# Kernel tuning notes

Measured on AMD Instinct MI355X. Metric: run time of the kernel, lower is better.

The kernel has to match this reference:

```python
import jax, jax.numpy as jnp
import numpy as np

H = 128   # hidden_size
E = 300   # embedding_dim
VOC = 32000
B, TP, TC = 8, 160, 160
D2 = 2 * H  # bidirectional feature dim


def gru_dir(x, Wih, Whh, bih, bhh, reverse):
    # x: [B,T,I] -> hidden states [B,T,Hs]; torch GRU gate order (r,z,n)
    Hs = Whh.shape[1]
    xg = jnp.einsum('bti,gi->btg', x, Wih) + bih  # [B,T,3Hs]
    if reverse:
        xg = xg[:, ::-1]
    def step(h, xt):
        gh = h @ Whh.T + bhh
        xr, xz, xn = jnp.split(xt, 3, axis=-1)
        hr, hz, hn = jnp.split(gh, 3, axis=-1)
        r = jax.nn.sigmoid(xr + hr)
        z = jax.nn.sigmoid(xz + hz)
        n = jnp.tanh(xn + r * hn)
        h = (1.0 - z) * n + z * h
        return h, h
    h0 = jnp.zeros((x.shape[0], Hs), x.dtype)
    _, hs = jax.lax.scan(step, h0, jnp.swapaxes(xg, 0, 1))
    hs = jnp.swapaxes(hs, 0, 1)
    if reverse:
        hs = hs[:, ::-1]
    return hs


def bigru(x, Wf, Uf, bif, bhf, Wb, Ub, bib, bhb):
    return jnp.concatenate([
        gru_dir(x, Wf, Uf, bif, bhf, False),
        gru_dir(x, Wb, Ub, bib, bhb, True)], axis=-1)


def setup_inputs() -> dict:
    key = jax.random.key(0)
    ks = iter(jax.random.split(key, 64))
    def rn(shape, s=0.05):
        return jax.random.normal(next(ks), shape, jnp.float32) * s
    inp = {}
    inp['text_a'] = jax.random.randint(next(ks), (B, TP), 0, VOC)
    inp['text_b'] = jax.random.randint(next(ks), (B, TC), 0, VOC)
    inp['emb'] = rn((VOC, E), 0.1)
    for pfx, ins in [('p', E), ('c', E), ('a', 6 * D2)]:
        for d in ('f', 'b'):
            inp[pfx + '_Wih_' + d] = rn((3 * H, ins))
            inp[pfx + '_Whh_' + d] = rn((3 * H, H))
            inp[pfx + '_bih_' + d] = jnp.zeros((3 * H,), jnp.float32)
            inp[pfx + '_bhh_' + d] = jnp.zeros((3 * H,), jnp.float32)
    inp['Wc1'] = rn((H, D2)); inp['Wc2'] = rn((H, D2)); inp['Vc'] = rn((H,))
    inp['Wb'] = rn((D2, D2))
    inp['Wd'] = rn((H, D2)); inp['Vd'] = rn((H,))
    inp['Wm'] = rn((H, D2)); inp['Vm'] = rn((H,))
    inp['Ws'] = rn((H, D2)); inp['Vs'] = rn((H,))
    inp['Wp'] = rn((H, D2)); inp['Vp'] = rn((H,))
    inp['W1'] = rn((H, D2)); inp['W2'] = rn((H, D2)); inp['Vv'] = rn((H,))
    inp['Wout'] = rn((2, D2)); inp['bout'] = jnp.zeros((2,), jnp.float32)
    return inp


def _forward(text_a, text_b, emb,
             p_Wih_f, p_Whh_f, p_bih_f, p_bhh_f, p_Wih_b, p_Whh_b, p_bih_b, p_bhh_b,
             c_Wih_f, c_Whh_f, c_bih_f, c_bhh_f, c_Wih_b, c_Whh_b, c_bih_b, c_bhh_b,
             a_Wih_f, a_Whh_f, a_bih_f, a_bhh_f, a_Wih_b, a_Whh_b, a_bih_b, a_bhh_b,
             Wc1, Wc2, Vc, Wb, Wd, Vd, Wm, Vm, Ws, Vs, Wp, Vp, W1, W2, Vv, Wout, bout):
    hp = bigru(emb[text_a], p_Wih_f, p_Whh_f, p_bih_f, p_bhh_f,
               p_Wih_b, p_Whh_b, p_bih_b, p_bhh_b)          # [B,Tp,2H]
    hc = bigru(emb[text_b], c_Wih_f, c_Whh_f, c_bih_f, c_bhh_f,
               c_Wih_b, c_Whh_b, c_bih_b, c_bhh_b)          # [B,Tc,2H]
    # concat (additive) attention: [B,Tc,Tp,H]
    s = jnp.tanh((hp @ Wc1.T)[:, None] + (hc @ Wc2.T)[:, :, None])
    a_cat = jax.nn.softmax(s @ Vc, axis=2)                   # [B,Tc,Tp]
    concat_rep = jnp.einsum('bct,btd->bcd', a_cat, hp)
    # bilinear attention
    a_bil = jax.nn.softmax(jnp.einsum('bcd,btd->bct', hc, hp @ Wb.T), axis=2)
    bil_rep = jnp.einsum('bct,btd->bcd', a_bil, hp)
    # dot / minus attention on [B,Tc,Tp,2H] broadcasts
    hp4 = hp[:, None]; hc4 = hc[:, :, None]
    a_dot = jax.nn.softmax(jnp.tanh((hp4 * hc4) @ Wd.T) @ Vd, axis=2)
    dot_rep = jnp.einsum('bct,btd->bcd', a_dot, hp)
    a_min = jax.nn.softmax(jnp.tanh((hp4 - hc4) @ Wm.T) @ Vm, axis=2)
    minus_rep = jnp.einsum('bct,btd->bcd', a_min, hp)
    # self attention on hc: [B,Tc,Tc,2H]
    a_self = jax.nn.softmax(jnp.tanh((hc[:, None] * hc[:, :, None]) @ Ws.T) @ Vs, axis=2)
    self_rep = jnp.einsum('bct,btd->bcd', a_self, hc)
    agg_in = jnp.concatenate([hc, self_rep, concat_rep, dot_rep, bil_rep, minus_rep], axis=-1)
    agg = bigru(agg_in, a_Wih_f, a_Whh_f, a_bih_f, a_bhh_f,
                a_Wih_b, a_Whh_b, a_bih_b, a_bhh_b)          # [B,Tc,2H]
    # pooled passage rep
    ap = jax.nn.softmax(jnp.tanh(hp @ Wp.T) @ Vp, axis=-1)   # [B,Tp]
    rp = jnp.einsum('bt,btd->bd', ap, hp)                    # [B,2H]
    # final attention over aggregation (note: no tanh, faithful to source)
    sc = (agg @ W1.T + (rp @ W2.T)[:, None]) @ Vv            # [B,Tc]
    ac = jax.nn.softmax(sc, axis=-1)
    rc = jnp.einsum('bc,bcd->bd', ac, agg)                   # [B,2H]
    return rc @ Wout.T + bout                                # [B,2] logits


def reference(text_a, text_b, emb,
              p_Wih_f, p_Whh_f, p_bih_f, p_bhh_f, p_Wih_b, p_Whh_b, p_bih_b, p_bhh_b,
              c_Wih_f, c_Whh_f, c_bih_f, c_bhh_f, c_Wih_b, c_Whh_b, c_bih_b, c_bhh_b,
              a_Wih_f, a_Whh_f, a_bih_f, a_bhh_f, a_Wih_b, a_Whh_b, a_bih_b, a_bhh_b,
              Wc1, Wc2, Vc, Wb, Wd, Vd, Wm, Vm, Ws, Vs, Wp, Vp, W1, W2, Vv, Wout, bout):
    return _forward(text_a, text_b, emb,
                    p_Wih_f, p_Whh_f, p_bih_f, p_bhh_f, p_Wih_b, p_Whh_b, p_bih_b, p_bhh_b,
                    c_Wih_f, c_Whh_f, c_bih_f, c_bhh_f, c_Wih_b, c_Whh_b, c_bih_b, c_bhh_b,
                    a_Wih_f, a_Whh_f, a_bih_f, a_bhh_f, a_Wih_b, a_Whh_b, a_bih_b, a_bhh_b,
                    Wc1, Wc2, Vc, Wb, Wd, Vd, Wm, Vm, Ws, Vs, Wp, Vp, W1, W2, Vv, Wout, bout)
```

## Files before the change

### kernel.cpp

```cpp
#include <hip/hip_runtime.h>

#define BB 8
#define TT 160
#define EE 300
#define HH 128
#define D2 256
#define G3 384
#define PSTR 40
#define HBP 900

typedef __attribute__((ext_vector_type(8))) short bf16x8;
typedef __attribute__((ext_vector_type(4))) float floatx4;

__device__ inline float fsigmoid(float x){ return 1.f/(1.f+__expf(-x)); }
__device__ inline float ftanh(float x){ return 2.f*fsigmoid(2.f*x) - 1.f; }

__device__ inline void split2(float x, unsigned short& hi, unsigned short& lo){
  unsigned ux = __float_as_uint(x);
  hi = (unsigned short)(ux>>16);
  float r = x - __uint_as_float(ux & 0xFFFF0000u);
  lo = (unsigned short)(__float_as_uint(r)>>16);
}

__device__ inline float quad_sum(float x){
  x += __uint_as_float(__builtin_amdgcn_mov_dpp(__float_as_uint(x), 0xB1, 0xF, 0xF, true));
  x += __uint_as_float(__builtin_amdgcn_mov_dpp(__float_as_uint(x), 0x4E, 0xF, 0xF, true));
  return x;
}

__global__ __launch_bounds__(256) void k_embed(const int* ta, const int* tb,
    const float* emb, float* ep, float* ec){
  const int idx = blockIdx.x*256 + threadIdx.x;
  const int per = BB*TT*EE;
  if (idx < per){
    const int e = idx % EE, bt = idx / EE;
    ep[idx] = emb[(long)ta[bt]*EE + e];
  } else {
    const int j = idx - per;
    const int e = j % EE, bt = j / EE;
    ec[j] = emb[(long)tb[bt]*EE + e];
  }
}

__global__ __launch_bounds__(256) void k_splitarr(const float* a, const float* b, int n,
    unsigned short* ahi, unsigned short* alo, unsigned short* bhi, unsigned short* blo){
  const int idx = blockIdx.x*256 + threadIdx.x;
  if (idx < n){
    split2(a[idx], ahi[idx], alo[idx]);
    split2(b[idx], bhi[idx], blo[idx]);
  }
}

struct SplitJob { const float* W; unsigned short* hi; unsigned short* lo; int n; int K; int Kp; };
struct SplitJobs { SplitJob j[14]; };

__global__ __launch_bounds__(256) void k_splitw(SplitJobs jobs){
  const SplitJob J = jobs.j[blockIdx.z];
  const int idx = blockIdx.x*256 + threadIdx.x;
  if (idx >= J.n) return;
  const int row = idx / J.Kp, k = idx - row*J.Kp;
  const float v = (k < J.K) ? J.W[(long)row*J.K + k] : 0.f;
  split2(v, J.hi[idx], J.lo[idx]);
}

struct GemmSJob {
  const float* A; const unsigned short* Whi; const unsigned short* Wlo; const float* bias;
  float* C; int N; int K; int Kp;
};
struct GemmSJobs { GemmSJob j[6]; };

__global__ __launch_bounds__(256) void k_gemmS(GemmSJobs jobs){
  const GemmSJob J = jobs.j[blockIdx.z];
  const int tid = threadIdx.x;
  const int lane = tid & 63, w = tid >> 6;
  const int l15 = lane & 15, q = lane >> 4;
  const int n0 = blockIdx.x * 64;
  if (n0 >= J.N) return;
  const int K = J.K, Kp = J.Kp;
  const long mrow = blockIdx.y*64 + w*16 + l15;
  const float* Arow = J.A + mrow*K;
  floatx4 acc[4];
  #pragma unroll
  for (int t=0;t<4;t++) acc[t] = (floatx4)0.f;
  const int nch = (K+31)>>5;
  for (int kc=0; kc<nch; kc++){
    const int k0 = kc<<5;
    const int kb = k0 + q*8;
    float av[8];
    if (k0+32 <= K){
      const floatx4 a0 = *(const floatx4*)(Arow+kb);
      const floatx4 a1 = *(const floatx4*)(Arow+kb+4);
      av[0]=a0[0];av[1]=a0[1];av[2]=a0[2];av[3]=a0[3];
      av[4]=a1[0];av[5]=a1[1];av[6]=a1[2];av[7]=a1[3];
    } else {
      #pragma unroll
      for (int j=0;j<8;j++){ const int k=kb+j; av[j] = (k<K)? Arow[k] : 0.f; }
    }
    union { bf16x8 v; unsigned short u[8]; } ahi, alo;
    #pragma unroll
    for (int j=0;j<8;j++) split2(av[j], ahi.u[j], alo.u[j]);
    #pragma unroll
    for (int t=0;t<4;t++){
      const int n = n0 + t*16 + l15;
      const long wo = (long)n*Kp + kb;
      union { bf16x8 v; uint4 d; } whi, wlo;
      whi.d = *(const uint4*)(J.Whi + wo);
      wlo.d = *(const uint4*)(J.Wlo + wo);
      acc[t] = __builtin_amdgcn_mfma_f32_16x16x32_bf16(ahi.v, whi.v, acc[t], 0,0,0);
      acc[t] = __builtin_amdgcn_mfma_f32_16x16x32_bf16(ahi.v, wlo.v, acc[t], 0,0,0);
      acc[t] = __builtin_amdgcn_mfma_f32_16x16x32_bf16(alo.v, whi.v, acc[t], 0,0,0);
    }
  }
  const long rbase = blockIdx.y*64 + w*16 + q*4;
  #pragma unroll
  for (int t=0;t<4;t++){
    const int n = n0 + t*16 + l15;
    const float bv = J.bias ? J.bias[n] : 0.f;
    #pragma unroll
    for (int r=0;r<4;r++)
      J.C[(rbase+r)*(long)J.N + n] = acc[t][r] + bv;
  }
}

struct GemmPJob {
  const unsigned short* Ahi; const unsigned short* Alo;
  const unsigned short* Whi; const unsigned short* Wlo; const float* bias;
  float* C; int N; int Kp;
};
struct GemmPJobs { GemmPJob j[6]; };

__global__ __launch_bounds__(256) void k_gemmSS(GemmPJobs jobs){
  const GemmPJob J = jobs.j[blockIdx.z];
  const int tid = threadIdx.x;
  const int lane = tid & 63, w = tid >> 6;
  const int l15 = lane & 15, q = lane >> 4;
  const int n0 = blockIdx.x * 64;
  if (n0 >= J.N) return;
  const int Kp = J.Kp;
  const long arow = (blockIdx.y*64 + w*16 + l15) * (long)Kp;
  floatx4 acc[4];
  #pragma unroll
  for (int t=0;t<4;t++) acc[t] = (floatx4)0.f;
  const int nch = Kp >> 5;
  for (int kc=0; kc<nch; kc++){
    const int kb = (kc<<5) + q*8;
    union { bf16x8 v; uint4 d; } ahi, alo;
    ahi.d = *(const uint4*)(J.Ahi + arow + kb);
    alo.d = *(const uint4*)(J.Alo + arow + kb);
    #pragma unroll
    for (int t=0;t<4;t++){
      const int n = n0 + t*16 + l15;
      const long wo = (long)n*Kp + kb;
      union { bf16x8 v; uint4 d; } whi, wlo;
      whi.d = *(const uint4*)(J.Whi + wo);
      wlo.d = *(const uint4*)(J.Wlo + wo);
      acc[t] = __builtin_amdgcn_mfma_f32_16x16x32_bf16(ahi.v, whi.v, acc[t], 0,0,0);
      acc[t] = __builtin_amdgcn_mfma_f32_16x16x32_bf16(ahi.v, wlo.v, acc[t], 0,0,0);
      acc[t] = __builtin_amdgcn_mfma_f32_16x16x32_bf16(alo.v, whi.v, acc[t], 0,0,0);
    }
  }
  const long rbase = blockIdx.y*64 + w*16 + q*4;
  #pragma unroll
  for (int t=0;t<4;t++){
    const int n = n0 + t*16 + l15;
    const float bv = J.bias ? J.bias[n] : 0.f;
    #pragma unroll
    for (int r=0;r<4;r++)
      J.C[(rbase+r)*(long)J.N + n] = acc[t][r] + bv;
  }
}

struct GruJob { const float* xg; const float* Whh; const float* bhh; float* out; int ocol; int rev; };
struct GruJobs { GruJob j[4]; };

__global__ __launch_bounds__(512,1) void k_gru(GruJobs jobs){
  const GruJob J = jobs.j[blockIdx.y];
  const int bi = blockIdx.x;
  const int tid = threadIdx.x;
  const int j = tid >> 2, p = tid & 3;
  const int rot = p*8;
  const int base = p*32;
  __shared__ float xgt[16][G3];
  __shared__ float hbuf[16][HBP];
  __shared__ float hcur[2][HH];
  const float* r0 = J.Whh + (long)j*HH + base;
  const float* z0 = J.Whh + (long)(HH+j)*HH + base;
  const float* n0 = J.Whh + (long)(2*HH+j)*HH + base;
  #define LDV(gp,i) (*(const floatx4*)((gp) + (((i)*4 + rot) & 31)))
  floatx4 wr0=LDV(r0,0), wr1=LDV(r0,1), wr2=LDV(r0,2), wr3=LDV(r0,3),
          wr4=LDV(r0,4), wr5=LDV(r0,5), wr6=LDV(r0,6), wr7=LDV(r0,7);
  floatx4 wz0=LDV(z0,0), wz1=LDV(z0,1), wz2=LDV(z0,2), wz3=LDV(z0,3),
          wz4=LDV(z0,4), wz5=LDV(z0,5), wz6=LDV(z0,6), wz7=LDV(z0,7);
  floatx4 wn0=LDV(n0,0), wn1=LDV(n0,1), wn2=LDV(n0,2), wn3=LDV(n0,3),
          wn4=LDV(n0,4), wn5=LDV(n0,5), wn6=LDV(n0,6), wn7=LDV(n0,7);
  #undef LDV
  asm volatile("" : "+v"(wr0), "+v"(wr1), "+v"(wr2), "+v"(wr3));
  asm volatile("" : "+v"(wr4), "+v"(wr5), "+v"(wr6), "+v"(wr7));
  asm volatile("" : "+v"(wz0), "+v"(wz1), "+v"(wz2), "+v"(wz3));
  asm volatile("" : "+v"(wz4), "+v"(wz5), "+v"(wz6), "+v"(wz7));
  asm volatile("" : "+v"(wn0), "+v"(wn1), "+v"(wn2), "+v"(wn3));
  asm volatile("" : "+v"(wn4), "+v"(wn5), "+v"(wn6), "+v"(wn7));
  const float bhr = J.bhh[j];
  const float bhz = J.bhh[HH+j];
  const float bhn = J.bhh[2*HH+j];
  if (tid < 256) ((float*)hcur)[tid] = 0.f;
  float hreg = 0.f;
  __syncthreads();

  for (int s0=0; s0<TT; s0+=16){
    #pragma unroll
    for (int r=0;r<3;r++){
      const int i = r*512 + tid;
      const int row = i/96, c4 = i - row*96;
      const int tt = J.rev ? (TT-1-(s0+row)) : (s0+row);
      *(floatx4*)&xgt[row][c4*4] = *(const floatx4*)(J.xg + ((long)bi*TT + tt)*G3 + c4*4);
    }
    __syncthreads();
    for (int si=0; si<16; si++){
      const int s = s0 + si;
      const int buf = s & 1;
      float ar=0.f, az=0.f, an=0.f;
      #define ACC(i) { \
        const floatx4 h4 = *(const floatx4*)&hcur[buf][base + (((i)*4 + rot) & 31)]; \
        ar += wr##i[0]*h4[0] + wr##i[1]*h4[1] + wr##i[2]*h4[2] + wr##i[3]*h4[3]; \
        az += wz##i[0]*h4[0] + wz##i[1]*h4[1] + wz##i[2]*h4[2] + wz##i[3]*h4[3]; \
        an += wn##i[0]*h4[0] + wn##i[1]*h4[1] + wn##i[2]*h4[2] + wn##i[3]*h4[3]; }
      ACC(0) ACC(1) ACC(2) ACC(3) ACC(4) ACC(5) ACC(6) ACC(7)
      #undef ACC
      const float cxr = xgt[si][j];
      const float cxz = xgt[si][HH+j];
      const float cxn = xgt[si][2*HH+j];
      ar = quad_sum(ar);
      az = quad_sum(az);
      an = quad_sum(an);
      const float gr = fsigmoid(cxr + ar + bhr);
      const float gz = fsigmoid(cxz + az + bhz);
      const float gn = ftanh  (cxn + gr*(an + bhn));
      const float h = (1.f-gz)*gn + gz*hreg;
      hreg = h;
      if (p==0){
        hcur[1-buf][j] = h;
        hbuf[si][j] = h;
      }
      __syncthreads();
    }
    {
      const int row = tid >> 5, c4 = tid & 31;
      const int tt = J.rev ? (TT-1-(s0+row)) : (s0+row);
      *(floatx4*)(J.out + ((long)bi*TT + tt)*D2 + J.ocol + c4*4) = *(const floatx4*)&hbuf[row][c4*4];
    }
  }
}

__device__ inline float block_softmax160(float s, int tid, float* red){
  float m = s;
  #pragma unroll
  for (int o=32;o>0;o>>=1) m = fmaxf(m, __shfl_xor(m,o));
  if ((tid&63)==0) red[tid>>6] = m;
  __syncthreads();
  m = fmaxf(fmaxf(red[0],red[1]), fmaxf(red[2],red[3]));
  const float p = (tid<TT) ? __expf(s-m) : 0.f;
  float t = p;
  #pragma unroll
  for (int o=32;o>0;o>>=1) t += __shfl_xor(t,o);
  if ((tid&63)==0) red[4+(tid>>6)] = t;
  __syncthreads();
  const float sum = red[4]+red[5]+red[6]+red[7];
  return p / sum;
}

struct PairJob { const unsigned short* Phi; const unsigned short* Plo;
                 const float* Q; const float* W; const float* V; float* a_out; };

__global__ __launch_bounds__(512) void k_pairattn(PairJob j0, PairJob j1){
  const PairJob J = blockIdx.z ? j1 : j0;
  const int b = blockIdx.y, c0 = blockIdx.x*2;
  const int tid = threadIdx.x;
  const int lane = tid & 63, w = tid >> 6;
  const int l15 = lane & 15, q = lane >> 4;
  __shared__ unsigned short Pb[2*2*160*PSTR];
  __shared__ float Qs[2][D2];
  __shared__ float sc_sh[2][TT];
  __shared__ float red[16];
  {
    const int row = tid >> 8, col = tid & 255;
    Qs[row][col] = J.Q[((long)b*TT + c0 + row)*D2 + col];
  }
  if (tid < 2*TT) ((float*)sc_sh)[tid] = 0.f;
  const long pbase = (long)b*TT*D2;

  const unsigned short* srcp[5];
  unsigned short* dstp[5];
  #pragma unroll
  for (int r=0;r<5;r++){
    const int idx = tid + r*512;
    const int hl = (idx >= 1280) ? 1 : 0;
    const int e4 = idx - hl*1280;
    const int st = e4 >> 3, sd4 = e4 & 7;
    srcp[r] = (hl ? J.Plo : J.Phi) + pbase + (long)st*D2 + sd4*4;
    dstp[r] = &Pb[((0*2 + hl)*160 + st)*PSTR + sd4*4];
  }
  uint2 stg[5];
  #pragma unroll
  for (int r=0;r<5;r++) stg[r] = *(const uint2*)(srcp[r]);
  const float* Wbase = J.W + (long)(w*16 + l15)*D2;
  floatx4 wv0 = *(const floatx4*)(Wbase + q*8);
  floatx4 wv1 = *(const floatx4*)(Wbase + q*8 + 4);
  #pragma unroll
  for (int r=0;r<5;r++) *(uint2*)(dstp[r]) = stg[r];
  __syncthreads();

  floatx4 acc0[10], acc1[10];
  #pragma unroll
  for (int nt=0;nt<10;nt++){ acc0[nt] = (floatx4)0.f; acc1[nt] = (floatx4)0.f; }

  for (int kc=0; kc<8; kc++){
    const floatx4 wc0 = wv0, wc1 = wv1;
    if (kc < 7){
      wv0 = *(const floatx4*)(Wbase + (kc+1)*32 + q*8);
      wv1 = *(const floatx4*)(Wbase + (kc+1)*32 + q*8 + 4);
      #pragma unroll
      for (int r=0;r<5;r++) stg[r] = *(const uint2*)(srcp[r] + (kc+1)*32);
    }
    const int d0 = kc*32 + q*8;
    const floatx4 q00 = *(const floatx4*)&Qs[0][d0];
    const floatx4 q01 = *(const floatx4*)&Qs[0][d0+4];
    const floatx4 q10 = *(const floatx4*)&Qs[1][d0];
    const floatx4 q11 = *(const floatx4*)&Qs[1][d0+4];
    union { bf16x8 v; unsigned short u[8]; } ah0, al0, ah1, al1;
    #pragma unroll
    for (int j=0;j<4;j++){
      split2(wc0[j]*q00[j], ah0.u[j],   al0.u[j]);
      split2(wc1[j]*q01[j], ah0.u[4+j], al0.u[4+j]);
      split2(wc0[j]*q10[j], ah1.u[j],   al1.u[j]);
      split2(wc1[j]*q11[j], ah1.u[4+j], al1.u[4+j]);
    }
    const int buf = kc & 1;
    #pragma unroll
    for (int nt=0;nt<10;nt++){
      const int t = nt*16 + l15;
      union { bf16x8 v; } bh, bl;
      bh.v = *(const bf16x8*)&Pb[((buf*2+0)*160 + t)*PSTR + q*8];
      bl.v = *(const bf16x8*)&Pb[((buf*2+1)*160 + t)*PSTR + q*8];
      acc0[nt] = __builtin_amdgcn_mfma_f32_16x16x32_bf16(ah0.v, bh.v, acc0[nt], 0,0,0);
      acc0[nt] = __builtin_amdgcn_mfma_f32_16x16x32_bf16(ah0.v, bl.v, acc0[nt], 0,0,0);
      acc0[nt] = __builtin_amdgcn_mfma_f32_16x16x32_bf16(al0.v, bh.v, acc0[nt], 0,0,0);
      acc1[nt] = __builtin_amdgcn_mfma_f32_16x16x32_bf16(ah1.v, bh.v, acc1[nt], 0,0,0);
      acc1[nt] = __builtin_amdgcn_mfma_f32_16x16x32_bf16(ah1.v, bl.v, acc1[nt], 0,0,0);
      acc1[nt] = __builtin_amdgcn_mfma_f32_16x16x32_bf16(al1.v, bh.v, acc1[nt], 0,0,0);
    }
    if (kc < 7){
      const int nbuf = 1 - buf;
      #pragma unroll
      for (int r=0;r<5;r++) *(uint2*)(dstp[r] + nbuf*(2*160*PSTR)) = stg[r];
      __syncthreads();
    }
  }

  float vreg[4];
  #pragma unroll
  for (int r=0;r<4;r++) vreg[r] = J.V[w*16 + q*4 + r];
  #pragma unroll
  for (int nt=0;nt<10;nt++){
    float p0 = 0.f, p1 = 0.f;
    #pragma unroll
    for (int r=0;r<4;r++){
      p0 += vreg[r]*ftanh(acc0[nt][r]);
      p1 += vreg[r]*ftanh(acc1[nt][r]);
    }
    p0 += __shfl_xor(p0,16); p0 += __shfl_xor(p0,32);
    p1 += __shfl_xor(p1,16); p1 += __shfl_xor(p1,32);
    if (q==0){
      atomicAdd(&sc_sh[0][nt*16 + l15], p0);
      atomicAdd(&sc_sh[1][nt*16 + l15], p1);
    }
  }
  __syncthreads();
  {
    const int row = tid >> 8, t_ = tid & 255;
    float s = (t_ < TT) ? sc_sh[row][t_] : -INFINITY;
    float m = s;
    #pragma unroll
    for (int o=32;o>0;o>>=1) m = fmaxf(m, __shfl_xor(m,o));
    if (lane==0) red[w] = m;
    __syncthreads();
    m = fmaxf(fmaxf(red[row*4+0],red[row*4+1]), fmaxf(red[row*4+2],red[row*4+3]));
    const float p = (t_ < TT) ? __expf(s-m) : 0.f;
    float su = p;
    #pragma unroll
    for (int o=32;o>0;o>>=1) su += __shfl_xor(su,o);
    if (lane==0) red[8+w] = su;
    __syncthreads();
    const float ssum = red[8+row*4+0]+red[8+row*4+1]+red[8+row*4+2]+red[8+row*4+3];
    if (t_ < TT) J.a_out[((long)b*TT + c0 + row)*TT + t_] = p/ssum;
  }
}

struct AddJob { const float* up; const float* uc; const float* V; float sgn; float* a_out; };

__global__ __launch_bounds__(256) void k_addattn(AddJob j0, AddJob j1){
  const AddJob J = blockIdx.z ? j1 : j0;
  const int b = blockIdx.y, c0 = blockIdx.x*16, tid = threadIdx.x;
  const int ci = tid >> 4, tj = tid & 15;
  __shared__ float ucc[16][132];
  __shared__ float up_sh[16][132];
  __shared__ float vv[HH];
  __shared__ float sc[16][TT];
  if (tid < HH) vv[tid] = J.V[tid];
  for (int i = tid; i < 16*HH; i += 256){
    const int cc = i >> 7, k = i & 127;
    ucc[cc][k] = J.sgn * J.uc[((long)b*TT + c0 + cc)*HH + k];
  }
  __syncthreads();
  for (int tch = 0; tch < 10; tch++){
    for (int i = tid; i < 16*HH; i += 256){
      const int tt = i >> 7, k = i & 127;
      up_sh[tt][k] = J.up[((long)b*TT + tch*16 + tt)*HH + k];
    }
    __syncthreads();
    float a0 = 0.f;
    #pragma unroll 4
    for (int k = 0; k < HH; k += 4){
      const floatx4 u4 = *(const floatx4*)&up_sh[tj][k];
      const floatx4 c4 = *(const floatx4*)&ucc[ci][k];
      a0 += vv[k]*ftanh(u4[0]+c4[0]) + vv[k+1]*ftanh(u4[1]+c4[1])
          + vv[k+2]*ftanh(u4[2]+c4[2]) + vv[k+3]*ftanh(u4[3]+c4[3]);
    }
    sc[ci][tch*16 + tj] = a0;
    __syncthreads();
  }
  float m = -INFINITY;
  float sv[10];
  #pragma unroll
  for (int u = 0; u < 10; u++){ sv[u] = sc[ci][tj + 16*u]; m = fmaxf(m, sv[u]); }
  #pragma unroll
  for (int o = 8; o >= 1; o >>= 1) m = fmaxf(m, __shfl_xor(m, o));
  float ssum = 0.f;
  #pragma unroll
  for (int u = 0; u < 10; u++){ sv[u] = __expf(sv[u] - m); ssum += sv[u]; }
  #pragma unroll
  for (int o = 8; o >= 1; o >>= 1) ssum += __shfl_xor(ssum, o);
  const float inv = 1.f / ssum;
  float* ao = J.a_out + ((long)b*TT + c0 + ci)*TT + tj;
  #pragma unroll
  for (int u = 0; u < 10; u++) ao[16*u] = sv[u]*inv;
}

__global__ __launch_bounds__(256) void k_bilattn(const float* hc, const float* hpWb, float* a_out){
  const int b = blockIdx.y, c = blockIdx.x, tid = threadIdx.x;
  __shared__ float hcc[D2];
  __shared__ float red[8];
  if (tid < D2) hcc[tid] = hc[((long)b*TT + c)*D2 + tid];
  __syncthreads();
  float s = -INFINITY;
  if (tid < TT){
    const float* pr = hpWb + ((long)b*TT + tid)*D2;
    float a0 = 0.f;
    #pragma unroll 4
    for (int k=0;k<D2;k++) a0 += hcc[k]*pr[k];
    s = a0;
  }
  const float a = block_softmax160(s, tid, red);
  if (tid < TT) a_out[((long)b*TT + c)*TT + tid] = a;
}

__global__ __launch_bounds__(256) void k_rep(const float* hp, const float* hc,
    const float* acat, const float* abil, const float* adot, const float* amin, const float* aself,
    float* aggin){
  const int b = blockIdx.y, c = blockIdx.x, tid = threadIdx.x;
  __shared__ float a5[5][TT];
  {
    const long base = ((long)b*TT + c)*TT;
    for (int i=tid;i<5*TT;i+=256){
      const int which = i/TT, t = i - which*TT;
      const float* p = which==0? acat : which==1? abil : which==2? adot : which==3? amin : aself;
      a5[which][t] = p[base + t];
    }
  }
  __syncthreads();
  const float* hpb = hp + (long)b*TT*D2 + tid;
  const float* hcb = hc + (long)b*TT*D2 + tid;
  float r0=0.f,r1=0.f,r2=0.f,r3=0.f,r4=0.f;
  for (int t=0;t<TT;t++){
    const float vp = hpb[(long)t*D2];
    const float vc = hcb[(long)t*D2];
    r0 += a5[0][t]*vp;
    r1 += a5[1][t]*vp;
    r2 += a5[2][t]*vp;
    r3 += a5[3][t]*vp;
    r4 += a5[4][t]*vc;
  }
  float* o = aggin + ((long)b*TT + c)*(6*D2);
  o[tid]        = hc[((long)b*TT + c)*D2 + tid];
  o[D2 + tid]   = r4;
  o[2*D2 + tid] = r0;
  o[3*D2 + tid] = r2;
  o[4*D2 + tid] = r1;
  o[5*D2 + tid] = r3;
}

__global__ __launch_bounds__(256) void k_tail1(const float* upP, const float* Vp,
    const float* hp, float* rp){
  const int b = blockIdx.x, tid = threadIdx.x;
  __shared__ float vv[HH];
  __shared__ float ap_sh[TT];
  __shared__ float red[8];
  if (tid<HH) vv[tid] = Vp[tid];
  __syncthreads();
  float s = -INFINITY;
  if (tid<TT){
    const float* ur = upP + ((long)b*TT + tid)*HH;
    float a0=0.f;
    #pragma unroll 4
    for (int k=0;k<HH;k++) a0 += vv[k]*ftanh(ur[k]);
    s = a0;
  }
  const float a = block_softmax160(s, tid, red);
  if (tid<TT) ap_sh[tid] = a;
  __syncthreads();
  float acc = 0.f;
  const float* hpb = hp + (long)b*TT*D2 + tid;
  for (int t=0;t<TT;t++) acc += ap_sh[t]*hpb[(long)t*D2];
  rp[b*D2 + tid] = acc;
}

__global__ __launch_bounds__(256) void k_tail2(const float* aggW1, const float* agg, const float* rp,
    const float* W2, const float* Vv, const float* Wout, const float* bout,
    float* out){
  const int b = blockIdx.x, tid = threadIdx.x;
  __shared__ float rps[D2];
  __shared__ float rpw[HH];
  __shared__ float ac_sh[TT];
  __shared__ float rc_sh[D2];
  __shared__ float red[8];
  if (tid < D2) rps[tid] = rp[b*D2 + tid];
  __syncthreads();
  if (tid < HH){
    float a0=0.f;
    const float* wr2 = W2 + (long)tid*D2;
    for (int d=0; d<D2; d+=4){
      const floatx4 w4 = *(const floatx4*)(wr2 + d);
      a0 += w4[0]*rps[d] + w4[1]*rps[d+1] + w4[2]*rps[d+2] + w4[3]*rps[d+3];
    }
    rpw[tid] = a0;
  }
  __syncthreads();
  float s = -INFINITY;
  if (tid < TT){
    const float* ar = aggW1 + ((long)b*TT + tid)*HH;
    float a0=0.f;
    for (int k=0;k<HH;k++) a0 += Vv[k]*(ar[k] + rpw[k]);
    s = a0;
  }
  const float a = block_softmax160(s, tid, red);
  if (tid < TT) ac_sh[tid] = a;
  __syncthreads();
  float rc=0.f;
  const float* ab = agg + (long)b*TT*D2 + tid;
  for (int t=0;t<TT;t++) rc += ac_sh[t]*ab[(long)t*D2];
  rc_sh[tid] = rc;
  __syncthreads();
  if (tid < 2){
    float o = bout[tid];
    const float* wr = Wout + (long)tid*D2;
    for (int d=0; d<D2; d++) o += wr[d]*rc_sh[d];
    out[b*2 + tid] = o;
  }
}

extern "C" void kernel_launch(void* const* d_in, const int* in_sizes, int n_in,
                              void* d_out, int out_size, void* d_ws, size_t ws_size,
                              hipStream_t stream){
  (void)in_sizes; (void)n_in; (void)out_size; (void)ws_size;
  const int* ta = (const int*)d_in[0];
  const int* tb = (const int*)d_in[1];
  const float* emb = (const float*)d_in[2];
  #define F32(i) ((const float*)d_in[i])

  float* ws = (float*)d_ws;
  float* ep    = ws;
  float* ec    = ep    + 384000;
  float* xg_pf = ec    + 384000;
  float* xg_pb = xg_pf + 491520;
  float* xg_cf = xg_pb + 491520;
  float* xg_cb = xg_cf + 491520;
  float* hp    = xg_cb + 491520;
  float* hc    = hp    + 327680;
  float* up1   = hc    + 327680;
  float* uc2   = up1   + 163840;
  float* ump   = uc2   + 163840;
  float* umc   = ump   + 163840;
  float* upP   = umc   + 163840;
  float* hpWb  = upP   + 163840;
  float* acat  = hpWb  + 327680;
  float* abil  = acat  + 204800;
  float* adot  = abil  + 204800;
  float* amin  = adot  + 204800;
  float* aself = amin  + 204800;
  float* aggin = aself + 204800;
  float* rp    = aggin + 1966080;
  unsigned short* hp_hi = (unsigned short*)(rp + 2048);
  unsigned short* hp_lo = hp_hi + 327680;
  unsigned short* hc_hi = hp_lo + 327680;
  unsigned short* hc_lo = hc_hi + 327680;
  unsigned short* wsp = hc_lo + 327680;
  unsigned short* w3h  = wsp;             unsigned short* w3l  = w3h  + 122880;
  unsigned short* w7h  = w3l  + 122880;   unsigned short* w7l  = w7h  + 122880;
  unsigned short* w11h = w7l  + 122880;   unsigned short* w11l = w11h + 122880;
  unsigned short* w15h = w11l + 122880;   unsigned short* w15l = w15h + 122880;
  unsigned short* w27h = w15l + 122880;   unsigned short* w27l = w27h + 32768;
  unsigned short* w28h = w27l + 32768;    unsigned short* w28l = w28h + 32768;
  unsigned short* w33h = w28l + 32768;    unsigned short* w33l = w33h + 32768;
  unsigned short* w37h = w33l + 32768;    unsigned short* w37l = w37h + 32768;
  unsigned short* w30h = w37l + 32768;    unsigned short* w30l = w30h + 65536;
  unsigned short* w19h = w30l + 65536;    unsigned short* w19l = w19h + 589824;
  unsigned short* w23h = w19l + 589824;   unsigned short* w23l = w23h + 589824;
  unsigned short* w39h = w23l + 589824;   unsigned short* w39l = w39h + 32768;
  unsigned short* eph  = w39l + 32768;    unsigned short* epl  = eph + 409600;
  unsigned short* ech  = epl + 409600;    unsigned short* ecl  = ech + 409600;
  unsigned short* agh  = (unsigned short*)up1;
  unsigned short* agl  = agh + 1966080;
  float* xg_af = xg_pf;
  float* xg_ab = xg_pb;
  float* agg   = xg_cf;
  float* aggW1 = xg_cb;

  k_embed<<<dim3(3000), dim3(256), 0, stream>>>(ta, tb, emb, ep, ec);
  SplitJobs sj = {};
  sj.j[0]  = {F32(3),  w3h,  w3l,  122880, 300, 320};
  sj.j[1]  = {F32(7),  w7h,  w7l,  122880, 300, 320};
  sj.j[2]  = {F32(11), w11h, w11l, 122880, 300, 320};
  sj.j[3]  = {F32(15), w15h, w15l, 122880, 300, 320};
  sj.j[4]  = {F32(27), w27h, w27l, 32768,  256, 256};
  sj.j[5]  = {F32(28), w28h, w28l, 32768,  256, 256};
  sj.j[6]  = {F32(33), w33h, w33l, 32768,  256, 256};
  sj.j[7]  = {F32(37), w37h, w37l, 32768,  256, 256};
  sj.j[8]  = {F32(30), w30h, w30l, 65536,  256, 256};
  sj.j[9]  = {F32(19), w19h, w19l, 589824, 1536, 1536};
  sj.j[10] = {F32(23), w23h, w23l, 589824, 1536, 1536};
  sj.j[11] = {F32(39), w39h, w39l, 32768,  256, 256};
  sj.j[12] = {ep,      eph,  epl,  409600, 300, 320};
  sj.j[13] = {ec,      ech,  ecl,  409600, 300, 320};
  k_splitw<<<dim3(2304,1,14), dim3(256), 0, stream>>>(sj);

  GemmPJobs ja = {};
  ja.j[0] = {eph, epl, w3h,  w3l,  F32(5),  xg_pf, 384, 320};
  ja.j[1] = {eph, epl, w7h,  w7l,  F32(9),  xg_pb, 384, 320};
  ja.j[2] = {ech, ecl, w11h, w11l, F32(13), xg_cf, 384, 320};
  ja.j[3] = {ech, ecl, w15h, w15l, F32(17), xg_cb, 384, 320};
  k_gemmSS<<<dim3(6,20,4), dim3(256), 0, stream>>>(ja);

  GruJobs gj = {};
  gj.j[0] = {xg_pf, F32(4),  F32(6),  hp, 0,   0};
  gj.j[1] = {xg_pb, F32(8),  F32(10), hp, 128, 1};
  gj.j[2] = {xg_cf, F32(12), F32(14), hc, 0,   0};
  gj.j[3] = {xg_cb, F32(16), F32(18), hc, 128, 1};
  k_gru<<<dim3(8,4), dim3(512), 0, stream>>>(gj);

  k_splitarr<<<dim3(1280), dim3(256), 0, stream>>>(hp, hc, 327680, hp_hi, hp_lo, hc_hi, hc_lo);

  GemmPJobs jb = {};
  jb.j[0] = {hp_hi, hp_lo, w27h, w27l, nullptr, up1,  128, 256};
  jb.j[1] = {hc_hi, hc_lo, w28h, w28l, nullptr, uc2,  128, 256};
  jb.j[2] = {hp_hi, hp_lo, w33h, w33l, nullptr, ump,  128, 256};
  jb.j[3] = {hc_hi, hc_lo, w33h, w33l, nullptr, umc,  128, 256};
  jb.j[4] = {hp_hi, hp_lo, w37h, w37l, nullptr, upP,  128, 256};
  jb.j[5] = {hp_hi, hp_lo, w30h, w30l, nullptr, hpWb, 256, 256};
  k_gemmSS<<<dim3(4,20,6), dim3(256), 0, stream>>>(jb);

  PairJob pd  = {hp_hi, hp_lo, hc, F32(31), F32(32), adot};
  PairJob psf = {hc_hi, hc_lo, hc, F32(35), F32(36), aself};
  k_pairattn<<<dim3(80,8,2), dim3(512), 0, stream>>>(pd, psf);

  AddJob ac_ = {up1, uc2, F32(29),  1.f, acat};
  AddJob am_ = {ump, umc, F32(34), -1.f, amin};
  k_addattn<<<dim3(10,8,2), dim3(256), 0, stream>>>(ac_, am_);

  k_bilattn<<<dim3(160,8), dim3(256), 0, stream>>>(hc, hpWb, abil);

  k_tail1<<<dim3(8), dim3(256), 0, stream>>>(upP, F32(38), hp, rp);

  k_rep<<<dim3(160,8), dim3(256), 0, stream>>>(hp, hc, acat, abil, adot, amin, aself, aggin);

  SplitJobs sja = {};
  sja.j[0] = {aggin, agh, agl, 1966080, 1536, 1536};
  k_splitw<<<dim3(7680,1,1), dim3(256), 0, stream>>>(sja);

  GemmPJobs jc = {};
  jc.j[0] = {agh, agl, w19h, w19l, F32(21), xg_af, 384, 1536};
  jc.j[1] = {agh, agl, w23h, w23l, F32(25), xg_ab, 384, 1536};
  k_gemmSS<<<dim3(6,20,2), dim3(256), 0, stream>>>(jc);

  GruJobs gja = {};
  gja.j[0] = {xg_af, F32(20), F32(22), agg, 0,   0};
  gja.j[1] = {xg_ab, F32(24), F32(26), agg, 128, 1};
  k_gru<<<dim3(8,2), dim3(512), 0, stream>>>(gja);

  GemmSJobs jd = {};
  jd.j[0] = {agg, w39h, w39l, nullptr, aggW1, 128, 256, 256};
  k_gemmS<<<dim3(2,20,1), dim3(256), 0, stream>>>(jd);

  k_tail2<<<dim3(8), dim3(256), 0, stream>>>(aggW1, agg, rp, F32(40), F32(41), F32(42), F32(43),
                                             (float*)d_out);
  #undef F32
}
```

Measured before the change: 821.1 us.

## Run GRU recurrence on MFMA with split-bf16 weights, batching all sequences per block

The GRU recurrent matvec moves from per-thread fp32 FMAs, with one block per batch element, to bf16x3 split MFMA 16x16x32. One block now processes all 8 batch rows as an MFMA M-dimension padded to 16, and the hidden state is kept as hi/lo bf16 in LDS. Recurrent weights are pre-split in the existing split kernel, and the grid shrinks from 8x4 to 1x4 blocks. This removes redundant per-batch weight register loads and uses matrix cores, but it serialises all batches onto fewer CUs and wastes half the MFMA rows. It also adds uncoalesced per-step global loads of xg and a large dummy LDS pad that forces one block per CU.

```diff
diff --git a/kernel.cpp b/kernel.cpp
--- a/kernel.cpp
+++ b/kernel.cpp
@@ -7,7 +7,6 @@
 #define D2 256
 #define G3 384
 #define PSTR 40
-#define HBP 900
 
 typedef __attribute__((ext_vector_type(8))) short bf16x8;
 typedef __attribute__((ext_vector_type(4))) float floatx4;
@@ -20,12 +19,6 @@
   hi = (unsigned short)(ux>>16);
   float r = x - __uint_as_float(ux & 0xFFFF0000u);
   lo = (unsigned short)(__float_as_uint(r)>>16);
-}
-
-__device__ inline float quad_sum(float x){
-  x += __uint_as_float(__builtin_amdgcn_mov_dpp(__float_as_uint(x), 0xB1, 0xF, 0xF, true));
-  x += __uint_as_float(__builtin_amdgcn_mov_dpp(__float_as_uint(x), 0x4E, 0xF, 0xF, true));
-  return x;
 }
 
 __global__ __launch_bounds__(256) void k_embed(const int* ta, const int* tb,
@@ -52,7 +45,7 @@
 }
 
 struct SplitJob { const float* W; unsigned short* hi; unsigned short* lo; int n; int K; int Kp; };
-struct SplitJobs { SplitJob j[14]; };
+struct SplitJobs { SplitJob j[20]; };
 
 __global__ __launch_bounds__(256) void k_splitw(SplitJobs jobs){
   const SplitJob J = jobs.j[blockIdx.z];
@@ -170,85 +163,96 @@
   }
 }
 
-struct GruJob { const float* xg; const float* Whh; const float* bhh; float* out; int ocol; int rev; };
+struct GruJob { const float* xg; const unsigned short* whh; const unsigned short* whl;
+                const float* bhh; float* out; int ocol; int rev; };
 struct GruJobs { GruJob j[4]; };
 
 __global__ __launch_bounds__(512,1) void k_gru(GruJobs jobs){
   const GruJob J = jobs.j[blockIdx.y];
-  const int bi = blockIdx.x;
   const int tid = threadIdx.x;
-  const int j = tid >> 2, p = tid & 3;
-  const int rot = p*8;
-  const int base = p*32;
-  __shared__ float xgt[16][G3];
-  __shared__ float hbuf[16][HBP];
-  __shared__ float hcur[2][HH];
-  const float* r0 = J.Whh + (long)j*HH + base;
-  const float* z0 = J.Whh + (long)(HH+j)*HH + base;
-  const float* n0 = J.Whh + (long)(2*HH+j)*HH + base;
-  #define LDV(gp,i) (*(const floatx4*)((gp) + (((i)*4 + rot) & 31)))
-  floatx4 wr0=LDV(r0,0), wr1=LDV(r0,1), wr2=LDV(r0,2), wr3=LDV(r0,3),
-          wr4=LDV(r0,4), wr5=LDV(r0,5), wr6=LDV(r0,6), wr7=LDV(r0,7);
-  floatx4 wz0=LDV(z0,0), wz1=LDV(z0,1), wz2=LDV(z0,2), wz3=LDV(z0,3),
-          wz4=LDV(z0,4), wz5=LDV(z0,5), wz6=LDV(z0,6), wz7=LDV(z0,7);
-  floatx4 wn0=LDV(n0,0), wn1=LDV(n0,1), wn2=LDV(n0,2), wn3=LDV(n0,3),
-          wn4=LDV(n0,4), wn5=LDV(n0,5), wn6=LDV(n0,6), wn7=LDV(n0,7);
-  #undef LDV
-  asm volatile("" : "+v"(wr0), "+v"(wr1), "+v"(wr2), "+v"(wr3));
-  asm volatile("" : "+v"(wr4), "+v"(wr5), "+v"(wr6), "+v"(wr7));
-  asm volatile("" : "+v"(wz0), "+v"(wz1), "+v"(wz2), "+v"(wz3));
-  asm volatile("" : "+v"(wz4), "+v"(wz5), "+v"(wz6), "+v"(wz7));
-  asm volatile("" : "+v"(wn0), "+v"(wn1), "+v"(wn2), "+v"(wn3));
-  asm volatile("" : "+v"(wn4), "+v"(wn5), "+v"(wn6), "+v"(wn7));
-  const float bhr = J.bhh[j];
-  const float bhz = J.bhh[HH+j];
-  const float bhn = J.bhh[2*HH+j];
-  if (tid < 256) ((float*)hcur)[tid] = 0.f;
-  float hreg = 0.f;
-  __syncthreads();
-
-  for (int s0=0; s0<TT; s0+=16){
-    #pragma unroll
-    for (int r=0;r<3;r++){
-      const int i = r*512 + tid;
-      const int row = i/96, c4 = i - row*96;
-      const int tt = J.rev ? (TT-1-(s0+row)) : (s0+row);
-      *(floatx4*)&xgt[row][c4*4] = *(const floatx4*)(J.xg + ((long)bi*TT + tt)*G3 + c4*4);
+  const int w = tid >> 6;
+  const int lane = tid & 63;
+  const int l15 = lane & 15, q = lane >> 4;
+  const int j = w*16 + l15;
+  __shared__ __align__(16) unsigned short Hhi[2][16][136];
+  __shared__ __align__(16) unsigned short Hlo[2][16][136];
+  __shared__ float ldspad[16384];
+  if (tid == 0) ((volatile float*)ldspad)[0] = 0.f;
+  for (int i = tid; i < 2*16*136/2; i += 512){
+    ((unsigned*)Hhi)[i] = 0u;
+    ((unsigned*)Hlo)[i] = 0u;
+  }
+  const long jb0 = (long)j*128 + q*8;
+  #define LBV(p,g,kc) (*(const bf16x8*)((p) + (long)(g)*16384 + jb0 + (kc)*32))
+  bf16x8 h00=LBV(J.whh,0,0), h01=LBV(J.whh,0,1), h02=LBV(J.whh,0,2), h03=LBV(J.whh,0,3);
+  bf16x8 h10=LBV(J.whh,1,0), h11=LBV(J.whh,1,1), h12=LBV(J.whh,1,2), h13=LBV(J.whh,1,3);
+  bf16x8 h20=LBV(J.whh,2,0), h21=LBV(J.whh,2,1), h22=LBV(J.whh,2,2), h23=LBV(J.whh,2,3);
+  bf16x8 l00=LBV(J.whl,0,0), l01=LBV(J.whl,0,1), l02=LBV(J.whl,0,2), l03=LBV(J.whl,0,3);
+  bf16x8 l10=LBV(J.whl,1,0), l11=LBV(J.whl,1,1), l12=LBV(J.whl,1,2), l13=LBV(J.whl,1,3);
+  bf16x8 l20=LBV(J.whl,2,0), l21=LBV(J.whl,2,1), l22=LBV(J.whl,2,2), l23=LBV(J.whl,2,3);
+  #undef LBV
+  asm volatile("" : "+v"(h00), "+v"(h01), "+v"(h02), "+v"(h03));
+  asm volatile("" : "+v"(h10), "+v"(h11), "+v"(h12), "+v"(h13));
+  asm volatile("" : "+v"(h20), "+v"(h21), "+v"(h22), "+v"(h23));
+  asm volatile("" : "+v"(l00), "+v"(l01), "+v"(l02), "+v"(l03));
+  asm volatile("" : "+v"(l10), "+v"(l11), "+v"(l12), "+v"(l13));
+  asm volatile("" : "+v"(l20), "+v"(l21), "+v"(l22), "+v"(l23));
+  const float bhr = J.bhh[j], bhz = J.bhh[128+j], bhn = J.bhh[256+j];
+  float hprev[4] = {0.f,0.f,0.f,0.f};
+  __syncthreads();
+
+  for (int t=0; t<TT; t++){
+    const int buf = t & 1;
+    const int tt = J.rev ? (TT-1-t) : t;
+    float cx0[4], cx1[4], cx2[4];
+    if (q < 2){
+      #pragma unroll
+      for (int r=0;r<4;r++){
+        const long base = ((long)(q*4+r)*TT + tt)*G3 + j;
+        cx0[r] = J.xg[base];
+        cx1[r] = J.xg[base+128];
+        cx2[r] = J.xg[base+256];
+      }
+    }
+    const bf16x8 a0 = *(const bf16x8*)&Hhi[buf][l15][q*8];
+    const bf16x8 a1 = *(const bf16x8*)&Hhi[buf][l15][32 + q*8];
+    const bf16x8 a2 = *(const bf16x8*)&Hhi[buf][l15][64 + q*8];
+    const bf16x8 a3 = *(const bf16x8*)&Hhi[buf][l15][96 + q*8];
+    const bf16x8 c0 = *(const bf16x8*)&Hlo[buf][l15][q*8];
+    const bf16x8 c1 = *(const bf16x8*)&Hlo[buf][l15][32 + q*8];
+    const bf16x8 c2 = *(const bf16x8*)&Hlo[buf][l15][64 + q*8];
+    const bf16x8 c3 = *(const bf16x8*)&Hlo[buf][l15][96 + q*8];
+    floatx4 g0 = (floatx4)0.f, g1 = (floatx4)0.f, g2 = (floatx4)0.f;
+    #define MM(A,B,ACC) ACC = __builtin_amdgcn_mfma_f32_16x16x32_bf16(A, B, ACC, 0,0,0)
+    MM(a0,h00,g0); MM(a0,h10,g1); MM(a0,h20,g2);
+    MM(a0,l00,g0); MM(a0,l10,g1); MM(a0,l20,g2);
+    MM(c0,h00,g0); MM(c0,h10,g1); MM(c0,h20,g2);
+    MM(a1,h01,g0); MM(a1,h11,g1); MM(a1,h21,g2);
+    MM(a1,l01,g0); MM(a1,l11,g1); MM(a1,l21,g2);
+    MM(c1,h01,g0); MM(c1,h11,g1); MM(c1,h21,g2);
+    MM(a2,h02,g0); MM(a2,h12,g1); MM(a2,h22,g2);
+    MM(a2,l02,g0); MM(a2,l12,g1); MM(a2,l22,g2);
+    MM(c2,h02,g0); MM(c2,h12,g1); MM(c2,h22,g2);
+    MM(a3,h03,g0); MM(a3,h13,g1); MM(a3,h23,g2);
+    MM(a3,l03,g0); MM(a3,l13,g1); MM(a3,l23,g2);
+    MM(c3,h03,g0); MM(c3,h13,g1); MM(c3,h23,g2);
+    #undef MM
+    if (q < 2){
+      #pragma unroll
+      for (int r=0;r<4;r++){
+        const int b = q*4 + r;
+        const float gr = fsigmoid(cx0[r] + g0[r] + bhr);
+        const float gz = fsigmoid(cx1[r] + g1[r] + bhz);
+        const float gn = ftanh  (cx2[r] + gr*(g2[r] + bhn));
+        const float h = (1.f-gz)*gn + gz*hprev[r];
+        hprev[r] = h;
+        unsigned short hi, lo; split2(h, hi, lo);
+        Hhi[1-buf][b][j] = hi;
+        Hlo[1-buf][b][j] = lo;
+        J.out[((long)b*TT + tt)*D2 + J.ocol + j] = h;
+      }
     }
     __syncthreads();
-    for (int si=0; si<16; si++){
-      const int s = s0 + si;
-      const int buf = s & 1;
-      float ar=0.f, az=0.f, an=0.f;
-      #define ACC(i) { \
-        const floatx4 h4 = *(const floatx4*)&hcur[buf][base + (((i)*4 + rot) & 31)]; \
-        ar += wr##i[0]*h4[0] + wr##i[1]*h4[1] + wr##i[2]*h4[2] + wr##i[3]*h4[3]; \
-        az += wz##i[0]*h4[0] + wz##i[1]*h4[1] + wz##i[2]*h4[2] + wz##i[3]*h4[3]; \
-        an += wn##i[0]*h4[0] + wn##i[1]*h4[1] + wn##i[2]*h4[2] + wn##i[3]*h4[3]; }
-      ACC(0) ACC(1) ACC(2) ACC(3) ACC(4) ACC(5) ACC(6) ACC(7)
-      #undef ACC
-      const float cxr = xgt[si][j];
-      const float cxz = xgt[si][HH+j];
-      const float cxn = xgt[si][2*HH+j];
-      ar = quad_sum(ar);
-      az = quad_sum(az);
-      an = quad_sum(an);
-      const float gr = fsigmoid(cxr + ar + bhr);
-      const float gz = fsigmoid(cxz + az + bhz);
-      const float gn = ftanh  (cxn + gr*(an + bhn));
-      const float h = (1.f-gz)*gn + gz*hreg;
-      hreg = h;
-      if (p==0){
-        hcur[1-buf][j] = h;
-        hbuf[si][j] = h;
-      }
-      __syncthreads();
-    }
-    {
-      const int row = tid >> 5, c4 = tid & 31;
-      const int tt = J.rev ? (TT-1-(s0+row)) : (s0+row);
-      *(floatx4*)(J.out + ((long)bi*TT + tt)*D2 + J.ocol + c4*4) = *(const floatx4*)&hbuf[row][c4*4];
-    }
   }
 }
 
@@ -618,6 +622,12 @@
   unsigned short* w39h = w23l + 589824;   unsigned short* w39l = w39h + 32768;
   unsigned short* eph  = w39l + 32768;    unsigned short* epl  = eph + 409600;
   unsigned short* ech  = epl + 409600;    unsigned short* ecl  = ech + 409600;
+  unsigned short* gpfh = ecl + 409600;    unsigned short* gpfl = gpfh + 49152;
+  unsigned short* gpbh = gpfl + 49152;    unsigned short* gpbl = gpbh + 49152;
+  unsigned short* gcfh = gpbl + 49152;    unsigned short* gcfl = gcfh + 49152;
+  unsigned short* gcbh = gcfl + 49152;    unsigned short* gcbl = gcbh + 49152;
+  unsigned short* gafh = gcbl + 49152;    unsigned short* gafl = gafh + 49152;
+  unsigned short* gabh = gafl + 49152;    unsigned short* gabl = gabh + 49152;
   unsigned short* agh  = (unsigned short*)up1;
   unsigned short* agl  = agh + 1966080;
   float* xg_af = xg_pf;
@@ -641,7 +651,13 @@
   sj.j[11] = {F32(39), w39h, w39l, 32768,  256, 256};
   sj.j[12] = {ep,      eph,  epl,  409600, 300, 320};
   sj.j[13] = {ec,      ech,  ecl,  409600, 300, 320};
-  k_splitw<<<dim3(2304,1,14), dim3(256), 0, stream>>>(sj);
+  sj.j[14] = {F32(4),  gpfh, gpfl, 49152,  128, 128};
+  sj.j[15] = {F32(8),  gpbh, gpbl, 49152,  128, 128};
+  sj.j[16] = {F32(12), gcfh, gcfl, 49152,  128, 128};
+  sj.j[17] = {F32(16), gcbh, gcbl, 49152,  128, 128};
+  sj.j[18] = {F32(20), gafh, gafl, 49152,  128, 128};
+  sj.j[19] = {F32(24), gabh, gabl, 49152,  128, 128};
+  k_splitw<<<dim3(2304,1,20), dim3(256), 0, stream>>>(sj);
 
   GemmPJobs ja = {};
   ja.j[0] = {eph, epl, w3h,  w3l,  F32(5),  xg_pf, 384, 320};
@@ -651,11 +667,11 @@
   k_gemmSS<<<dim3(6,20,4), dim3(256), 0, stream>>>(ja);
 
   GruJobs gj = {};
-  gj.j[0] = {xg_pf, F32(4),  F32(6),  hp, 0,   0};
-  gj.j[1] = {xg_pb, F32(8),  F32(10), hp, 128, 1};
-  gj.j[2] = {xg_cf, F32(12), F32(14), hc, 0,   0};
-  gj.j[3] = {xg_cb, F32(16), F32(18), hc, 128, 1};
-  k_gru<<<dim3(8,4), dim3(512), 0, stream>>>(gj);
+  gj.j[0] = {xg_pf, gpfh, gpfl, F32(6),  hp, 0,   0};
+  gj.j[1] = {xg_pb, gpbh, gpbl, F32(10), hp, 128, 1};
+  gj.j[2] = {xg_cf, gcfh, gcfl, F32(14), hc, 0,   0};
+  gj.j[3] = {xg_cb, gcbh, gcbl, F32(18), hc, 128, 1};
+  k_gru<<<dim3(1,4), dim3(512), 0, stream>>>(gj);
 
   k_splitarr<<<dim3(1280), dim3(256), 0, stream>>>(hp, hc, 327680, hp_hi, hp_lo, hc_hi, hc_lo);
 
@@ -692,9 +708,9 @@
   k_gemmSS<<<dim3(6,20,2), dim3(256), 0, stream>>>(jc);
 
   GruJobs gja = {};
-  gja.j[0] = {xg_af, F32(20), F32(22), agg, 0,   0};
-  gja.j[1] = {xg_ab, F32(24), F32(26), agg, 128, 1};
-  k_gru<<<dim3(8,2), dim3(512), 0, stream>>>(gja);
+  gja.j[0] = {xg_af, gafh, gafl, F32(22), agg, 0,   0};
+  gja.j[1] = {xg_ab, gabh, gabl, F32(26), agg, 128, 1};
+  k_gru<<<dim3(1,2), dim3(512), 0, stream>>>(gja);
 
   GemmSJobs jd = {};
   jd.j[0] = {agg, w39h, w39l, nullptr, aggW1, 128, 256, 256};
```

Result: slower. 1.096 ms (+33.5%).
